# Optimization experiments

Hardware: AMD Instinct MI355X
Metric: run time of the kernel (lower is better)

The kernel has to match this reference:

```python
import jax, jax.numpy as jnp
import numpy as np

B, T = 256, 256
IN = [300, 74, 35]
H = [128, 32, 32]
TH = sum(H)            # 192 total hidden
ATT = 4                # attn_num
ACD = 64               # attn_cell_dim
COMP = [32, 16, 16]
ZDIM = sum(COMP)       # 64
CCD = [64, 32, 32]     # compression_cell_dims
OCD, OUT = 64, 1


def _mlp(x, w1, b1, w2, b2, act=None):
    # SimpleNet at inference: Linear -> ReLU -> (dropout=identity) -> Linear -> act
    o = jax.nn.relu(x @ w1 + b1) @ w2 + b2
    return act(o) if act is not None else o


def _lsthm(x, c, h, z, W, U, V, b, hd):
    s = x @ W + h @ U + z @ V + b  # [B, 4*hd]
    f = jax.nn.sigmoid(s[:, :hd])
    i = jax.nn.sigmoid(s[:, hd:2 * hd])
    o = jax.nn.sigmoid(s[:, 2 * hd:3 * hd])
    ch = jnp.tanh(s[:, 3 * hd:])
    c_t = f * c + i * ch
    h_t = jnp.tanh(c_t) * o
    return c_t, h_t


def setup_inputs() -> dict:
    key = jax.random.key(0)
    ks = iter(jax.random.split(key, 64))
    rn = lambda shape, s=0.05: jax.random.normal(next(ks), shape, dtype=jnp.float32) * s
    inp = {}
    for i, d in enumerate(IN):
        inp[f"x{i}"] = jax.random.normal(next(ks), (B, T, d), dtype=jnp.float32)
    for i in range(3):
        inp[f"W{i}"] = rn((IN[i], 4 * H[i]))
        inp[f"U{i}"] = rn((H[i], 4 * H[i]))
        inp[f"V{i}"] = rn((ZDIM, 4 * H[i]))
        inp[f"b{i}"] = jnp.zeros((4 * H[i],), jnp.float32)
    inp["aw1"] = rn((TH, ACD * ATT)); inp["ab1"] = jnp.zeros((ACD * ATT,), jnp.float32)
    inp["aw2"] = rn((ACD * ATT, TH * ATT)); inp["ab2"] = jnp.zeros((TH * ATT,), jnp.float32)
    for i in range(3):
        inp[f"cw1_{i}"] = rn((H[i] * ATT, CCD[i])); inp[f"cb1_{i}"] = jnp.zeros((CCD[i],), jnp.float32)
        inp[f"cw2_{i}"] = rn((CCD[i], COMP[i])); inp[f"cb2_{i}"] = jnp.zeros((COMP[i],), jnp.float32)
    inp["fw1"] = rn((ZDIM + TH, OCD)); inp["fb1"] = jnp.zeros((OCD,), jnp.float32)
    inp["fw2"] = rn((OCD, OUT)); inp["fb2"] = jnp.zeros((OUT,), jnp.float32)
    return inp


def reference(x0, x1, x2,
              W0, U0, V0, b0, W1, U1, V1, b1, W2, U2, V2, b2,
              aw1, ab1, aw2, ab2,
              cw1_0, cb1_0, cw2_0, cb2_0,
              cw1_1, cb1_1, cw2_1, cb2_1,
              cw1_2, cb1_2, cw2_2, cb2_2,
              fw1, fb1, fw2, fb2):
    b = x0.shape[0]
    init = (jnp.zeros((b, H[0]), x0.dtype), jnp.zeros((b, H[1]), x0.dtype), jnp.zeros((b, H[2]), x0.dtype),
            jnp.zeros((b, H[0]), x0.dtype), jnp.zeros((b, H[1]), x0.dtype), jnp.zeros((b, H[2]), x0.dtype),
            jnp.zeros((b, ZDIM), x0.dtype))
    s0 = H[0] * ATT
    s1 = s0 + H[1] * ATT

    def step(carry, xt):
        c0, c1, c2, h0, h1, h2, z = carry
        x0t, x1t, x2t = xt
        c0, h0 = _lsthm(x0t, c0, h0, z, W0, U0, V0, b0, H[0])
        c1, h1 = _lsthm(x1t, c1, h1, z, W1, U1, V1, b1, H[1])
        c2, h2 = _lsthm(x2t, c2, h2, z, W2, U2, V2, b2, H[2])
        hcat = jnp.concatenate([h0, h1, h2], axis=1)  # [B, TH]
        att = _mlp(hcat, aw1, ab1, aw2, ab2, jax.nn.sigmoid)  # [B, ATT*TH]
        atts = jax.nn.softmax(att.reshape(b, ATT, TH), axis=2).reshape(b, ATT * TH)
        out_tensor = jnp.concatenate([jnp.tile(h0, (1, ATT)), jnp.tile(h1, (1, ATT)), jnp.tile(h2, (1, ATT))], axis=1)
        att_out = atts * out_tensor
        d0 = _mlp(att_out[:, :s0], cw1_0, cb1_0, cw2_0, cb2_0, jax.nn.sigmoid)
        d1 = _mlp(att_out[:, s0:s1], cw1_1, cb1_1, cw2_1, cb2_1, jax.nn.sigmoid)
        d2 = _mlp(att_out[:, s1:], cw1_2, cb1_2, cw2_2, cb2_2, jax.nn.sigmoid)
        z = jax.nn.softmax(jnp.concatenate([d0, d1, d2], axis=1), axis=1)
        return (c0, c1, c2, h0, h1, h2, z), None

    xs = (jnp.swapaxes(x0, 0, 1), jnp.swapaxes(x1, 0, 1), jnp.swapaxes(x2, 0, 1))  # time-leading
    (c0, c1, c2, h0, h1, h2, z), _ = jax.lax.scan(step, init, xs)
    total = jnp.concatenate([z, h0, h1, h2], axis=1)  # [B, ZDIM+TH]
    return _mlp(total, fw1, fb1, fw2, fb2)  # [B, 1]
```

## Files before the change

### kernel.cpp

```cpp
#include <hip/hip_runtime.h>
#include <hip/hip_bf16.h>
#include <hip/hip_fp16.h>
#include <math.h>

#define BB 256
#define TT 256

__device__ __forceinline__ float sigf(float x) { return 1.f / (1.f + expf(-x)); }

typedef _Float16 half8v __attribute__((ext_vector_type(8)));
typedef _Float16 half2v __attribute__((ext_vector_type(2)));

__device__ __forceinline__ void dot8p(float (&acc)[8], float4 wv0, float4 wv1,
                                      float a0, float a1) {
#if __has_builtin(__builtin_amdgcn_fdot2)
    const half2v ap = __builtin_bit_cast(half2v, __builtin_amdgcn_cvt_pkrtz(a0, a1));
    acc[0] = __builtin_amdgcn_fdot2(__builtin_bit_cast(half2v, wv0.x), ap, acc[0], false);
    acc[1] = __builtin_amdgcn_fdot2(__builtin_bit_cast(half2v, wv0.y), ap, acc[1], false);
    acc[2] = __builtin_amdgcn_fdot2(__builtin_bit_cast(half2v, wv0.z), ap, acc[2], false);
    acc[3] = __builtin_amdgcn_fdot2(__builtin_bit_cast(half2v, wv0.w), ap, acc[3], false);
    acc[4] = __builtin_amdgcn_fdot2(__builtin_bit_cast(half2v, wv1.x), ap, acc[4], false);
    acc[5] = __builtin_amdgcn_fdot2(__builtin_bit_cast(half2v, wv1.y), ap, acc[5], false);
    acc[6] = __builtin_amdgcn_fdot2(__builtin_bit_cast(half2v, wv1.z), ap, acc[6], false);
    acc[7] = __builtin_amdgcn_fdot2(__builtin_bit_cast(half2v, wv1.w), ap, acc[7], false);
#else
    half8v h0 = __builtin_bit_cast(half8v, wv0);
    half8v h1 = __builtin_bit_cast(half8v, wv1);
#pragma unroll
    for (int m = 0; m < 4; ++m) acc[m]     += (float)h0[2*m] * a0 + (float)h0[2*m+1] * a1;
#pragma unroll
    for (int m = 0; m < 4; ++m) acc[4 + m] += (float)h1[2*m] * a0 + (float)h1[2*m+1] * a1;
#endif
}

#define BAR() do {                                   \
    __atomic_signal_fence(__ATOMIC_SEQ_CST);         \
    __builtin_amdgcn_s_waitcnt(0xC07F);              \
    __builtin_amdgcn_s_barrier();                    \
    __atomic_signal_fence(__ATOMIC_SEQ_CST);         \
} while (0)

__global__ void f2h_pair(const float* __restrict__ s, __half* __restrict__ d,
                         int K, int N) {
    int i = blockIdx.x * 256 + threadIdx.x;
    if (i < K * N) {
        int k = i / N, j = i - k * N;
        d[(size_t)(k >> 1) * (2 * N) + 2 * j + (k & 1)] = __float2half(s[i]);
    }
}

#define GT_M 128
#define GT_N 64
#define GT_K 16

__device__ __forceinline__ void stvec4(float* p, float4 v) { *(float4*)p = v; }
__device__ __forceinline__ void stvec4(__half* p, float4 v) {
    *(__half2*)p = __floats2half2_rn(v.x, v.y);
    *(__half2*)(p + 2) = __floats2half2_rn(v.z, v.w);
}

template <typename OT>
__global__ __launch_bounds__(256)
void xw_gemm(const float* __restrict__ X, const float* __restrict__ W,
             const float* __restrict__ bias, OT* __restrict__ G,
             int M, int N, int K) {
    __shared__ float As[GT_K][GT_M + 4];
    __shared__ float Bs[GT_K][GT_N];
    const int tid = threadIdx.x;
    const int bm = blockIdx.y * GT_M;
    const int bn = blockIdx.x * GT_N;
    const int tx = tid & 15;
    const int ty = tid >> 4;

    float acc[8][4];
#pragma unroll
    for (int i = 0; i < 8; ++i)
#pragma unroll
        for (int j = 0; j < 4; ++j) acc[i][j] = 0.f;

    for (int kt = 0; kt < K; kt += GT_K) {
#pragma unroll
        for (int i = 0; i < 8; ++i) {
            int idx = i * 256 + tid;
            int m = idx >> 4, k = idx & 15;
            int gk = kt + k;
            As[k][m] = (gk < K) ? X[(size_t)(bm + m) * K + gk] : 0.f;
        }
#pragma unroll
        for (int i = 0; i < 4; ++i) {
            int idx = i * 256 + tid;
            int k = idx >> 6, n = idx & 63;
            int gk = kt + k;
            Bs[k][n] = (gk < K) ? W[(size_t)gk * N + bn + n] : 0.f;
        }
        __syncthreads();
#pragma unroll
        for (int k = 0; k < GT_K; ++k) {
            float a[8], b[4];
            const float4 a0 = *(const float4*)&As[k][ty * 8];
            const float4 a1 = *(const float4*)&As[k][ty * 8 + 4];
            const float4 bv = *(const float4*)&Bs[k][tx * 4];
            a[0]=a0.x; a[1]=a0.y; a[2]=a0.z; a[3]=a0.w;
            a[4]=a1.x; a[5]=a1.y; a[6]=a1.z; a[7]=a1.w;
            b[0]=bv.x; b[1]=bv.y; b[2]=bv.z; b[3]=bv.w;
#pragma unroll
            for (int i = 0; i < 8; ++i)
#pragma unroll
                for (int j = 0; j < 4; ++j) acc[i][j] += a[i] * b[j];
        }
        __syncthreads();
    }
    const int n0 = bn + tx * 4;
#pragma unroll
    for (int i = 0; i < 8; ++i) {
        int m = bm + ty * 8 + i;
        float4 v;
        v.x = acc[i][0] + bias[n0 + 0];
        v.y = acc[i][1] + bias[n0 + 1];
        v.z = acc[i][2] + bias[n0 + 2];
        v.w = acc[i][3] + bias[n0 + 3];
        stvec4(&G[(size_t)m * N + n0], v);
    }
}

__global__ __launch_bounds__(512, 1)
void marn_rec(const float* __restrict__ G0, const __half* __restrict__ G1h,
              const __half* __restrict__ G2h,
              const __half* __restrict__ hU0, const __half* __restrict__ hV0,
              const __half* __restrict__ hU1, const __half* __restrict__ hV1,
              const __half* __restrict__ hU2, const __half* __restrict__ hV2,
              const __half* __restrict__ haw1, const float* __restrict__ ab1,
              const __half* __restrict__ haw2, const float* __restrict__ ab2,
              const __half* __restrict__ hcw10, const float* __restrict__ cb10,
              const float* __restrict__ cw20, const float* __restrict__ cb20,
              const __half* __restrict__ hcw11, const float* __restrict__ cb11,
              const float* __restrict__ cw21, const float* __restrict__ cb21,
              const __half* __restrict__ hcw12, const float* __restrict__ cb12,
              const float* __restrict__ cw22, const float* __restrict__ cb22,
              const float* __restrict__ fw1, const float* __restrict__ fb1,
              const float* __restrict__ fw2, const float* __restrict__ fb2,
              float* __restrict__ out) {
    __shared__ float hz[256];
    __shared__ float cst[192];
    __shared__ float a1s[256];
    __shared__ float attE[768];
    __shared__ float hid[128];
    __shared__ float rinv[4];
    __shared__ float scratch[3840];
    __shared__ float c2w[3072];
    __shared__ __align__(16) __half s_aw1[49152];
    __shared__ __align__(16) __half s_c1b[8192];

    const int tid = threadIdx.x;
    const int row = blockIdx.x;
    const int rotPA = ((row >> 3) & 3) * 4;
    const int rotPB = ((row >> 3) & 7) * 4;
    const int rotPC = ((row >> 3) & 3) * 4;

    for (int i = tid; i < 256; i += 512) hz[i] = 0.f;
    if (tid < 192) cst[tid] = 0.f;
    for (int i = tid; i < 2048; i += 512) c2w[i] = cw20[i];
    if (tid < 512) { c2w[2048 + tid] = cw21[tid]; c2w[2560 + tid] = cw22[tid]; }
    {
        const float4* s4 = (const float4*)haw1;
        float4* d4 = (float4*)s_aw1;
        for (int i = tid; i < 6144; i += 512) d4[i] = s4[i];
        float4* d1 = (float4*)s_c1b;
        d1[tid] = ((const float4*)hcw11)[tid];
        d1[512 + tid] = ((const float4*)hcw12)[tid];
    }
    __syncthreads();

    const __half* WBa = nullptr; int HOa = 0, STRa = 0, SOa = 0;
    if (tid < 384) {
        const int g = tid & 63, kc = tid >> 6;
        const int cb = g * 8;
        if (kc < 4) { WBa = hU0 + (size_t)(16 * kc) * 1024 + 2 * cb; HOa = 32 * kc; }
        else        { WBa = hV0 + (size_t)(16 * (kc - 4)) * 1024 + 2 * cb; HOa = 192 + 32 * (kc - 4); }
        STRa = 1024;
        SOa = kc * 512 + cb;
    } else if (tid < 480) {
        const int u = tid - 384;
        const int kc = u >> 5;
        const int g2 = u & 31;
        const int cell = g2 >> 4;
        const int cb = (g2 & 15) * 8;
        const __half* Uc = cell ? hU2 : hU1;
        const __half* Vc = cell ? hV2 : hV1;
        if (kc == 0) { WBa = Uc + 2 * cb; HOa = 128 + 32 * cell; }
        else         { WBa = Vc + (size_t)(16 * (kc - 1)) * 256 + 2 * cb; HOa = 192 + 32 * (kc - 1); }
        STRa = 256;
        SOa = 3072 + kc * 256 + cell * 128 + cb;
    }
    int AW1o = 0, HO1 = 0, SO1 = 0;
    if (tid < 256) {
        const int g = tid & 31, kc = tid >> 5;
        const int cb = g * 8;
        AW1o = kc * 6144 + 2 * cb;
        HO1 = 24 * kc;
        SO1 = kc * 256 + cb;
    }
    const int kc2 = tid / 96;
    const int g2a = tid - kc2 * 96;
    const __half* WB2 = haw2 + (size_t)(32 * kc2) * 1536 + 2 * (g2a * 8);
    const int HO2 = 64 * kc2;
    const int SO2 = kc2 * 768 + g2a * 8;
    const __half* WBc = nullptr; int HOc = 0, SOc = 0, C1o = 0, HSELo = 0, HSELm = 0, HBc = 0;
    if (tid < 128) {
        const int g = tid & 7, kc = tid >> 3;
        WBc = hcw10 + (size_t)(16 * kc) * 128 + 2 * (g * 8);
        HOc = 32 * kc;
        SOc = kc * 64 + g * 8;
        HSELo = 0; HSELm = 127; HBc = 0;
    } else if (tid < 192) {
        const int u = tid - 128;
        const int cell = u >> 5;
        const int rem = u & 31;
        const int g = rem & 3, kc = rem >> 2;
        C1o = cell * 4096 + kc * 512 + 2 * (g * 8);
        HOc = 512 + 128 * cell + 16 * kc;
        SOc = 1024 + cell * 256 + kc * 32 + g * 8;
        HSELo = 128 + 32 * cell; HSELm = 31; HBc = 512 + 128 * cell;
    }
    const int AHc = HOc / 192;
    const int g12_cell = ((tid - 128) >> 5) & 1;
    const int g12_uu   = (tid - 128) & 31;

    float  g0p[4];
    __half g12p[4];
    if (tid < 128) {
        const float* gp = G0 + ((size_t)row * TT + 0) * 512;
#pragma unroll
        for (int q = 0; q < 4; ++q) g0p[q] = gp[q * 128 + tid];
    } else if (tid < 192) {
        const __half* gp = (g12_cell ? G2h : G1h) + ((size_t)row * TT + 0) * 128;
#pragma unroll
        for (int q = 0; q < 4; ++q) g12p[q] = gp[q * 32 + g12_uu];
    }

    for (int t = 0; t < TT; ++t) {
        if (tid < 480) {
            float acc[8];
#pragma unroll
            for (int j = 0; j < 8; ++j) acc[j] = 0.f;
#pragma unroll 8
            for (int p = 0; p < 16; ++p) {
                const int kk = (p + rotPA) & 15;
                const __half* wp = WBa + (size_t)kk * STRa;
                dot8p(acc, *(const float4*)wp, *(const float4*)(wp + 8),
                      hz[HOa + 2 * kk], hz[HOa + 2 * kk + 1]);
            }
            float* s0 = &scratch[SOa];
            *(float4*)s0       = make_float4(acc[0], acc[1], acc[2], acc[3]);
            *(float4*)(s0 + 4) = make_float4(acc[4], acc[5], acc[6], acc[7]);
        }
        BAR();
        if (tid < 128) {
            float s[4];
#pragma unroll
            for (int q = 0; q < 4; ++q) {
                const int c4 = q * 128 + tid;
                float v = g0p[q];
#pragma unroll
                for (int kc = 0; kc < 6; ++kc) v += scratch[kc * 512 + c4];
                s[q] = v;
            }
            const float f  = sigf(s[0]);
            const float ig = sigf(s[1]);
            const float o  = sigf(s[2]);
            const float ch = tanhf(s[3]);
            const float c = f * cst[tid] + ig * ch;
            cst[tid] = c;
            hz[tid] = tanhf(c) * o;
        } else if (tid < 192) {
            const int cell = g12_cell, uu = g12_uu;
            float s[4];
#pragma unroll
            for (int q = 0; q < 4; ++q) {
                float v = __half2float(g12p[q]);
#pragma unroll
                for (int kc = 0; kc < 3; ++kc)
                    v += scratch[3072 + kc * 256 + cell * 128 + q * 32 + uu];
                s[q] = v;
            }
            const float f  = sigf(s[0]);
            const float ig = sigf(s[1]);
            const float o  = sigf(s[2]);
            const float ch = tanhf(s[3]);
            const int si = 128 + 32 * cell + uu;
            const float c = f * cst[si] + ig * ch;
            cst[si] = c;
            hz[si] = tanhf(c) * o;
        }
        BAR();
        if (tid < 256) {
            float acc[8];
#pragma unroll
            for (int j = 0; j < 8; ++j) acc[j] = 0.f;
            const __half* wp = &s_aw1[AW1o];
#pragma unroll
            for (int p = 0; p < 12; ++p)
                dot8p(acc, *(const float4*)(wp + p * 512), *(const float4*)(wp + p * 512 + 8),
                      hz[HO1 + 2 * p], hz[HO1 + 2 * p + 1]);
            float* s0 = &scratch[SO1];
            *(float4*)s0       = make_float4(acc[0], acc[1], acc[2], acc[3]);
            *(float4*)(s0 + 4) = make_float4(acc[4], acc[5], acc[6], acc[7]);
        }
        BAR();
        if (tid < 256) {
            float s = ab1[tid];
#pragma unroll
            for (int kc = 0; kc < 8; ++kc) s += scratch[kc * 256 + tid];
            a1s[tid] = fmaxf(s, 0.f);
        }
        BAR();
        if (tid < 384) {
            float acc[8];
#pragma unroll
            for (int j = 0; j < 8; ++j) acc[j] = 0.f;
#pragma unroll 8
            for (int p = 0; p < 32; ++p) {
                const int kk = (p + rotPB) & 31;
                const __half* wp = WB2 + (size_t)kk * 1536;
                dot8p(acc, *(const float4*)wp, *(const float4*)(wp + 8),
                      a1s[HO2 + 2 * kk], a1s[HO2 + 2 * kk + 1]);
            }
            float* s0 = &scratch[SO2];
            *(float4*)s0       = make_float4(acc[0], acc[1], acc[2], acc[3]);
            *(float4*)(s0 + 4) = make_float4(acc[4], acc[5], acc[6], acc[7]);
        }
        BAR();
#pragma unroll
        for (int i = 0; i < 2; ++i) {
            const int idx = i * 512 + tid;
            if (idx < 768) {
                float s = ab2[idx];
#pragma unroll
                for (int kc = 0; kc < 4; ++kc) s += scratch[kc * 768 + idx];
                attE[idx] = expf(sigf(s));
            }
        }
        BAR();
        if (tid < 256) {
            const int a = tid >> 6, lane = tid & 63;
            float v = attE[a * 192 + lane] + attE[a * 192 + 64 + lane]
                    + attE[a * 192 + 128 + lane];
#pragma unroll
            for (int s = 32; s >= 1; s >>= 1) v += __shfl_xor(v, s);
            if (lane == 0) rinv[a] = 1.f / v;
        }
        BAR();
        if (tid < 192) {
            const float ri = rinv[AHc];
            float acc[8];
#pragma unroll
            for (int j = 0; j < 8; ++j) acc[j] = 0.f;
            if (tid < 128) {
#pragma unroll 8
                for (int p = 0; p < 16; ++p) {
                    const int kk = (p + rotPC) & 15;
                    const int i0 = HOc + 2 * kk;
                    const float a0 = attE[i0] * ri * hz[i0 & 127];
                    const float a1 = attE[i0 + 1] * ri * hz[(i0 + 1) & 127];
                    const __half* wp = WBc + (size_t)kk * 128;
                    dot8p(acc, *(const float4*)wp, *(const float4*)(wp + 8), a0, a1);
                }
            } else {
                const __half* wp = &s_c1b[C1o];
#pragma unroll
                for (int p = 0; p < 8; ++p) {
                    const int i0 = HOc + 2 * p;
                    const float a0 = attE[i0] * ri * hz[HSELo + ((i0 - HBc) & HSELm)];
                    const float a1 = attE[i0 + 1] * ri * hz[HSELo + ((i0 + 1 - HBc) & HSELm)];
                    dot8p(acc, *(const float4*)(wp + p * 64), *(const float4*)(wp + p * 64 + 8),
                          a0, a1);
                }
            }
            float* s0 = &scratch[SOc];
            *(float4*)s0       = make_float4(acc[0], acc[1], acc[2], acc[3]);
            *(float4*)(s0 + 4) = make_float4(acc[4], acc[5], acc[6], acc[7]);
        }
        BAR();
        if (tid < 128) {
            float s;
            if (tid < 64) {
                s = cb10[tid];
#pragma unroll
                for (int kc = 0; kc < 16; ++kc) s += scratch[kc * 64 + tid];
            } else {
                const int cc = tid - 64;
                const int cell = cc >> 5, j = cc & 31;
                s = (cell ? cb12 : cb11)[j];
#pragma unroll
                for (int kc = 0; kc < 8; ++kc)
                    s += scratch[1024 + cell * 256 + kc * 32 + j];
            }
            hid[tid] = fmaxf(s, 0.f);
        }
        BAR();
        if (tid < 64) {
            const int j = tid;
            float acc;
            if (j < 32) {
                acc = cb20[j];
#pragma unroll
                for (int k = 0; k < 64; ++k) acc += hid[k] * c2w[k * 32 + j];
            } else if (j < 48) {
                const int o = j - 32; acc = cb21[o];
#pragma unroll
                for (int k = 0; k < 32; ++k) acc += hid[64 + k] * c2w[2048 + k * 16 + o];
            } else {
                const int o = j - 48; acc = cb22[o];
#pragma unroll
                for (int k = 0; k < 32; ++k) acc += hid[96 + k] * c2w[2560 + k * 16 + o];
            }
            const float e = expf(sigf(acc));
            float v = e;
#pragma unroll
            for (int s = 32; s >= 1; s >>= 1) v += __shfl_xor(v, s);
            hz[192 + j] = e / v;
        }
        {
            const int tn = (t + 1 < TT) ? t + 1 : TT - 1;
            if (tid < 128) {
                const float* gp = G0 + ((size_t)row * TT + tn) * 512;
#pragma unroll
                for (int q = 0; q < 4; ++q) g0p[q] = gp[q * 128 + tid];
            } else if (tid < 192) {
                const __half* gp = (g12_cell ? G2h : G1h) + ((size_t)row * TT + tn) * 128;
#pragma unroll
                for (int q = 0; q < 4; ++q) g12p[q] = gp[q * 32 + g12_uu];
            }
        }
        BAR();
    }

    __syncthreads();
    if (tid < 64) {
        const int j = tid;
        float acc = fb1[j];
#pragma unroll 8
        for (int k = 0; k < 64; ++k)  acc += hz[192 + k] * fw1[k * 64 + j];
#pragma unroll 8
        for (int k = 0; k < 192; ++k) acc += hz[k] * fw1[(64 + k) * 64 + j];
        hid[j] = fmaxf(acc, 0.f);
    }
    __syncthreads();
    if (tid < 64) {
        float v = hid[tid] * fw2[tid];
#pragma unroll
        for (int s = 32; s >= 1; s >>= 1) v += __shfl_xor(v, s);
        if (tid == 0) out[row] = v + fb2[0];
    }
}

extern "C" void kernel_launch(void* const* d_in, const int* in_sizes, int n_in,
                              void* d_out, int out_size, void* d_ws, size_t ws_size,
                              hipStream_t stream) {
    const float* x0   = (const float*)d_in[0];
    const float* x1   = (const float*)d_in[1];
    const float* x2   = (const float*)d_in[2];
    const float* W0   = (const float*)d_in[3];
    const float* U0   = (const float*)d_in[4];
    const float* V0   = (const float*)d_in[5];
    const float* b0   = (const float*)d_in[6];
    const float* W1   = (const float*)d_in[7];
    const float* U1   = (const float*)d_in[8];
    const float* V1   = (const float*)d_in[9];
    const float* b1   = (const float*)d_in[10];
    const float* W2   = (const float*)d_in[11];
    const float* U2   = (const float*)d_in[12];
    const float* V2   = (const float*)d_in[13];
    const float* b2   = (const float*)d_in[14];
    const float* aw1  = (const float*)d_in[15];
    const float* ab1  = (const float*)d_in[16];
    const float* aw2  = (const float*)d_in[17];
    const float* ab2  = (const float*)d_in[18];
    const float* cw10 = (const float*)d_in[19];
    const float* cb10 = (const float*)d_in[20];
    const float* cw20 = (const float*)d_in[21];
    const float* cb20 = (const float*)d_in[22];
    const float* cw11 = (const float*)d_in[23];
    const float* cb11 = (const float*)d_in[24];
    const float* cw21 = (const float*)d_in[25];
    const float* cb21 = (const float*)d_in[26];
    const float* cw12 = (const float*)d_in[27];
    const float* cb12 = (const float*)d_in[28];
    const float* cw22 = (const float*)d_in[29];
    const float* cb22 = (const float*)d_in[30];
    const float* fw1  = (const float*)d_in[31];
    const float* fb1  = (const float*)d_in[32];
    const float* fw2  = (const float*)d_in[33];
    const float* fb2  = (const float*)d_in[34];
    float* out = (float*)d_out;

    const size_t M = (size_t)BB * TT;

    float*  G0  = (float*)d_ws;
    __half* G1h = (__half*)(G0 + M * 512);
    __half* G2h = G1h + M * 128;
    __half* hU0   = G2h + M * 128;
    __half* hV0   = hU0 + 65536;
    __half* hU1   = hV0 + 32768;
    __half* hV1   = hU1 + 4096;
    __half* hU2   = hV1 + 8192;
    __half* hV2   = hU2 + 4096;
    __half* haw1  = hV2 + 8192;
    __half* haw2  = haw1 + 49152;
    __half* hcw10 = haw2 + 196608;
    __half* hcw11 = hcw10 + 32768;
    __half* hcw12 = hcw11 + 4096;

    f2h_pair<<<(65536 + 255) / 256, 256, 0, stream>>>(U0, hU0, 128, 512);
    f2h_pair<<<(32768 + 255) / 256, 256, 0, stream>>>(V0, hV0, 64, 512);
    f2h_pair<<<(4096 + 255) / 256, 256, 0, stream>>>(U1, hU1, 32, 128);
    f2h_pair<<<(8192 + 255) / 256, 256, 0, stream>>>(V1, hV1, 64, 128);
    f2h_pair<<<(4096 + 255) / 256, 256, 0, stream>>>(U2, hU2, 32, 128);
    f2h_pair<<<(8192 + 255) / 256, 256, 0, stream>>>(V2, hV2, 64, 128);
    f2h_pair<<<(49152 + 255) / 256, 256, 0, stream>>>(aw1, haw1, 192, 256);
    f2h_pair<<<(196608 + 255) / 256, 256, 0, stream>>>(aw2, haw2, 256, 768);
    f2h_pair<<<(32768 + 255) / 256, 256, 0, stream>>>(cw10, hcw10, 512, 64);
    f2h_pair<<<(4096 + 255) / 256, 256, 0, stream>>>(cw11, hcw11, 128, 32);
    f2h_pair<<<(4096 + 255) / 256, 256, 0, stream>>>(cw12, hcw12, 128, 32);

    xw_gemm<float><<<dim3(512 / GT_N, M / GT_M), 256, 0, stream>>>(x0, W0, b0, G0, (int)M, 512, 300);
    xw_gemm<__half><<<dim3(128 / GT_N, M / GT_M), 256, 0, stream>>>(x1, W1, b1, G1h, (int)M, 128, 74);
    xw_gemm<__half><<<dim3(128 / GT_N, M / GT_M), 256, 0, stream>>>(x2, W2, b2, G2h, (int)M, 128, 35);

    marn_rec<<<256, 512, 0, stream>>>(G0, G1h, G2h, hU0, hV0, hU1, hV1, hU2, hV2,
                                      haw1, ab1, haw2, ab2,
                                      hcw10, cb10, cw20, cb20,
                                      hcw11, cb11, cw21, cb21,
                                      hcw12, cb12, cw22, cb22,
                                      fw1, fb1, fw2, fb2, out);
}
```

Before: 3.202 ms.

## Overlap U0 recurrent matvec with attention stage and defer softmax normalization

Moves the h0·U0 partial products out of the first per-step phase and into the idle threads of the attention first-layer phase, storing them in a new shared buffer for the next step's gate sum. The softmax normalization is deferred: the compression layer uses unnormalized exponentials and the per-head reciprocal is applied afterward per k-chunk, which lets the row-sum reduction run concurrently with the compression matvec and removes one barrier per timestep. This costs extra shared memory and relies on each k-chunk mapping to exactly one attention head.

```diff
diff --git a/kernel.cpp b/kernel.cpp
--- a/kernel.cpp
+++ b/kernel.cpp
@@ -146,6 +146,7 @@
     __shared__ float attE[768];
     __shared__ float hid[128];
     __shared__ float rinv[4];
+    __shared__ float uhA[2048];
     __shared__ float scratch[3840];
     __shared__ float c2w[3072];
     __shared__ __align__(16) __half s_aw1[49152];
@@ -159,6 +160,7 @@
 
     for (int i = tid; i < 256; i += 512) hz[i] = 0.f;
     if (tid < 192) cst[tid] = 0.f;
+    for (int i = tid; i < 2048; i += 512) uhA[i] = 0.f;
     for (int i = tid; i < 2048; i += 512) c2w[i] = cw20[i];
     if (tid < 512) { c2w[2048 + tid] = cw21[tid]; c2w[2560 + tid] = cw22[tid]; }
     {
@@ -192,6 +194,12 @@
         STRa = 256;
         SOa = 3072 + kc * 256 + cell * 128 + cb;
     }
+    const int uj   = tid - 256;
+    const int ukc  = (uj >> 6) & 3;
+    const int ug   = uj & 63;
+    const __half* WBu = hU0 + (size_t)(16 * ukc) * 1024 + 2 * (ug * 8);
+    const int HOu = 32 * ukc;
+    const int UOu = ukc * 512 + ug * 8;
     int AW1o = 0, HO1 = 0, SO1 = 0;
     if (tid < 256) {
         const int g = tid & 31, kc = tid >> 5;
@@ -222,7 +230,6 @@
         SOc = 1024 + cell * 256 + kc * 32 + g * 8;
         HSELo = 128 + 32 * cell; HSELm = 31; HBc = 512 + 128 * cell;
     }
-    const int AHc = HOc / 192;
     const int g12_cell = ((tid - 128) >> 5) & 1;
     const int g12_uu   = (tid - 128) & 31;
 
@@ -239,7 +246,7 @@
     }
 
     for (int t = 0; t < TT; ++t) {
-        if (tid < 480) {
+        if (tid >= 256 && tid < 480) {
             float acc[8];
 #pragma unroll
             for (int j = 0; j < 8; ++j) acc[j] = 0.f;
@@ -262,7 +269,9 @@
                 const int c4 = q * 128 + tid;
                 float v = g0p[q];
 #pragma unroll
-                for (int kc = 0; kc < 6; ++kc) v += scratch[kc * 512 + c4];
+                for (int kc = 0; kc < 4; ++kc) v += uhA[kc * 512 + c4];
+#pragma unroll
+                for (int kc = 4; kc < 6; ++kc) v += scratch[kc * 512 + c4];
                 s[q] = v;
             }
             const float f  = sigf(s[0]);
@@ -305,6 +314,20 @@
             float* s0 = &scratch[SO1];
             *(float4*)s0       = make_float4(acc[0], acc[1], acc[2], acc[3]);
             *(float4*)(s0 + 4) = make_float4(acc[4], acc[5], acc[6], acc[7]);
+        } else {
+            float acc[8];
+#pragma unroll
+            for (int j = 0; j < 8; ++j) acc[j] = 0.f;
+#pragma unroll 8
+            for (int p = 0; p < 16; ++p) {
+                const int kk = (p + rotPA) & 15;
+                const __half* wp = WBu + (size_t)kk * 1024;
+                dot8p(acc, *(const float4*)wp, *(const float4*)(wp + 8),
+                      hz[HOu + 2 * kk], hz[HOu + 2 * kk + 1]);
+            }
+            float* s0 = &uhA[UOu];
+            *(float4*)s0       = make_float4(acc[0], acc[1], acc[2], acc[3]);
+            *(float4*)(s0 + 4) = make_float4(acc[4], acc[5], acc[6], acc[7]);
         }
         BAR();
         if (tid < 256) {
@@ -341,17 +364,7 @@
             }
         }
         BAR();
-        if (tid < 256) {
-            const int a = tid >> 6, lane = tid & 63;
-            float v = attE[a * 192 + lane] + attE[a * 192 + 64 + lane]
-                    + attE[a * 192 + 128 + lane];
-#pragma unroll
-            for (int s = 32; s >= 1; s >>= 1) v += __shfl_xor(v, s);
-            if (lane == 0) rinv[a] = 1.f / v;
-        }
-        BAR();
         if (tid < 192) {
-            const float ri = rinv[AHc];
             float acc[8];
 #pragma unroll
             for (int j = 0; j < 8; ++j) acc[j] = 0.f;
@@ -360,8 +373,8 @@
                 for (int p = 0; p < 16; ++p) {
                     const int kk = (p + rotPC) & 15;
                     const int i0 = HOc + 2 * kk;
-                    const float a0 = attE[i0] * ri * hz[i0 & 127];
-                    const float a1 = attE[i0 + 1] * ri * hz[(i0 + 1) & 127];
+                    const float a0 = attE[i0] * hz[i0 & 127];
+                    const float a1 = attE[i0 + 1] * hz[(i0 + 1) & 127];
                     const __half* wp = WBc + (size_t)kk * 128;
                     dot8p(acc, *(const float4*)wp, *(const float4*)(wp + 8), a0, a1);
                 }
@@ -370,8 +383,8 @@
 #pragma unroll
                 for (int p = 0; p < 8; ++p) {
                     const int i0 = HOc + 2 * p;
-                    const float a0 = attE[i0] * ri * hz[HSELo + ((i0 - HBc) & HSELm)];
-                    const float a1 = attE[i0 + 1] * ri * hz[HSELo + ((i0 + 1 - HBc) & HSELm)];
+                    const float a0 = attE[i0] * hz[HSELo + ((i0 - HBc) & HSELm)];
+                    const float a1 = attE[i0 + 1] * hz[HSELo + ((i0 + 1 - HBc) & HSELm)];
                     dot8p(acc, *(const float4*)(wp + p * 64), *(const float4*)(wp + p * 64 + 8),
                           a0, a1);
                 }
@@ -379,6 +392,14 @@
             float* s0 = &scratch[SOc];
             *(float4*)s0       = make_float4(acc[0], acc[1], acc[2], acc[3]);
             *(float4*)(s0 + 4) = make_float4(acc[4], acc[5], acc[6], acc[7]);
+        } else if (tid < 448) {
+            const int u = tid - 192;
+            const int a = u >> 6, lane = u & 63;
+            float v = attE[a * 192 + lane] + attE[a * 192 + 64 + lane]
+                    + attE[a * 192 + 128 + lane];
+#pragma unroll
+            for (int s = 32; s >= 1; s >>= 1) v += __shfl_xor(v, s);
+            if (lane == 0) rinv[a] = 1.f / v;
         }
         BAR();
         if (tid < 128) {
@@ -386,14 +407,16 @@
             if (tid < 64) {
                 s = cb10[tid];
 #pragma unroll
-                for (int kc = 0; kc < 16; ++kc) s += scratch[kc * 64 + tid];
+                for (int kc = 0; kc < 16; ++kc)
+                    s += scratch[kc * 64 + tid] * rinv[(32 * kc) / 192];
             } else {
                 const int cc = tid - 64;
                 const int cell = cc >> 5, j = cc & 31;
                 s = (cell ? cb12 : cb11)[j];
 #pragma unroll
                 for (int kc = 0; kc < 8; ++kc)
-                    s += scratch[1024 + cell * 256 + kc * 32 + j];
+                    s += scratch[1024 + cell * 256 + kc * 32 + j]
+                         * rinv[(512 + 128 * cell + 16 * kc) / 192];
             }
             hid[tid] = fmaxf(s, 0.f);
         }
```

New measurement: 3.257 ms. No clear change (+1.7%).

## Process two batch rows per block to reuse recurrent weight loads

Applied to the files above, without the earlier changes.

Each workgroup now handles two batch rows, duplicating hidden state, scratch and attention buffers, and each loaded weight vector feeds two accumulator sets. The grid is halved to 128 blocks. The aim is to halve per-row weight fetch bandwidth and put idle threads to work in the elementwise phases. The risk is longer per-timestep latency in a sequential recurrence and leaving half the CUs unused. The LDS copy of the small compression weights is also removed, so those are now read from global memory.

```diff
diff --git a/kernel.cpp b/kernel.cpp
--- a/kernel.cpp
+++ b/kernel.cpp
@@ -140,34 +140,31 @@
               const float* __restrict__ fw1, const float* __restrict__ fb1,
               const float* __restrict__ fw2, const float* __restrict__ fb2,
               float* __restrict__ out) {
-    __shared__ float hz[256];
-    __shared__ float cst[192];
-    __shared__ float a1s[256];
-    __shared__ float attE[768];
-    __shared__ float hid[128];
-    __shared__ float rinv[4];
-    __shared__ float scratch[3840];
+    __shared__ float hz[512];
+    __shared__ float cst[384];
+    __shared__ float a1s[512];
+    __shared__ float attE[1536];
+    __shared__ float hid[256];
+    __shared__ float rinv[8];
+    __shared__ float scratch[7680];
     __shared__ float c2w[3072];
     __shared__ __align__(16) __half s_aw1[49152];
-    __shared__ __align__(16) __half s_c1b[8192];
 
     const int tid = threadIdx.x;
-    const int row = blockIdx.x;
-    const int rotPA = ((row >> 3) & 3) * 4;
-    const int rotPB = ((row >> 3) & 7) * 4;
-    const int rotPC = ((row >> 3) & 3) * 4;
-
-    for (int i = tid; i < 256; i += 512) hz[i] = 0.f;
-    if (tid < 192) cst[tid] = 0.f;
+    const int bid = blockIdx.x;
+    const int row0 = 2 * bid;
+    const int rotPA = ((bid >> 3) & 3) * 4;
+    const int rotPB = ((bid >> 3) & 7) * 4;
+    const int rotPC = ((bid >> 3) & 3) * 4;
+
+    hz[tid] = 0.f;
+    if (tid < 384) cst[tid] = 0.f;
     for (int i = tid; i < 2048; i += 512) c2w[i] = cw20[i];
-    if (tid < 512) { c2w[2048 + tid] = cw21[tid]; c2w[2560 + tid] = cw22[tid]; }
+    { c2w[2048 + tid] = cw21[tid & 511]; c2w[2560 + tid] = cw22[tid & 511]; }
     {
         const float4* s4 = (const float4*)haw1;
         float4* d4 = (float4*)s_aw1;
         for (int i = tid; i < 6144; i += 512) d4[i] = s4[i];
-        float4* d1 = (float4*)s_c1b;
-        d1[tid] = ((const float4*)hcw11)[tid];
-        d1[512 + tid] = ((const float4*)hcw12)[tid];
     }
     __syncthreads();
 
@@ -192,108 +189,122 @@
         STRa = 256;
         SOa = 3072 + kc * 256 + cell * 128 + cb;
     }
-    int AW1o = 0, HO1 = 0, SO1 = 0;
-    if (tid < 256) {
-        const int g = tid & 31, kc = tid >> 5;
-        const int cb = g * 8;
-        AW1o = kc * 6144 + 2 * cb;
+    const int lt = tid & 255;
+    const int rr = tid >> 8;
+    int AW1o, HO1, SO1;
+    {
+        const int g = lt & 31, kc = lt >> 5;
+        AW1o = kc * 6144 + 2 * (g * 8);
         HO1 = 24 * kc;
-        SO1 = kc * 256 + cb;
+        SO1 = kc * 256 + g * 8;
     }
     const int kc2 = tid / 96;
     const int g2a = tid - kc2 * 96;
     const __half* WB2 = haw2 + (size_t)(32 * kc2) * 1536 + 2 * (g2a * 8);
     const int HO2 = 64 * kc2;
     const int SO2 = kc2 * 768 + g2a * 8;
-    const __half* WBc = nullptr; int HOc = 0, SOc = 0, C1o = 0, HSELo = 0, HSELm = 0, HBc = 0;
+    const __half* WBc = nullptr; const __half* WC1 = nullptr;
+    int HOc = 0, SOc = 0, HSELo = 0, HSELm = 0, HBc = 0, AHc = 0, c1row = 0;
     if (tid < 128) {
         const int g = tid & 7, kc = tid >> 3;
         WBc = hcw10 + (size_t)(16 * kc) * 128 + 2 * (g * 8);
         HOc = 32 * kc;
         SOc = kc * 64 + g * 8;
-        HSELo = 0; HSELm = 127; HBc = 0;
-    } else if (tid < 192) {
-        const int u = tid - 128;
+        AHc = HOc / 192;
+    } else if (tid < 256) {
+        const int u = (tid - 128) & 63;
+        c1row = (tid - 128) >> 6;
         const int cell = u >> 5;
         const int rem = u & 31;
         const int g = rem & 3, kc = rem >> 2;
-        C1o = cell * 4096 + kc * 512 + 2 * (g * 8);
+        WC1 = (cell ? hcw12 : hcw11) + kc * 512 + 2 * (g * 8);
         HOc = 512 + 128 * cell + 16 * kc;
         SOc = 1024 + cell * 256 + kc * 32 + g * 8;
         HSELo = 128 + 32 * cell; HSELm = 31; HBc = 512 + 128 * cell;
-    }
-    const int AHc = HOc / 192;
-    const int g12_cell = ((tid - 128) >> 5) & 1;
-    const int g12_uu   = (tid - 128) & 31;
+        AHc = HOc / 192;
+    }
+    const bool gBig   = (tid < 128) || (tid >= 256 && tid < 384);
+    const bool gSmall = (lt >= 128 && lt < 192);
+    const int  gC     = tid & 127;
+    const int  sCell  = ((lt - 128) >> 5) & 1;
+    const int  sUU    = (lt - 128) & 31;
 
     float  g0p[4];
     __half g12p[4];
-    if (tid < 128) {
-        const float* gp = G0 + ((size_t)row * TT + 0) * 512;
-#pragma unroll
-        for (int q = 0; q < 4; ++q) g0p[q] = gp[q * 128 + tid];
-    } else if (tid < 192) {
-        const __half* gp = (g12_cell ? G2h : G1h) + ((size_t)row * TT + 0) * 128;
-#pragma unroll
-        for (int q = 0; q < 4; ++q) g12p[q] = gp[q * 32 + g12_uu];
+    if (gBig) {
+        const float* gp = G0 + ((size_t)(row0 + rr) * TT + 0) * 512;
+#pragma unroll
+        for (int q = 0; q < 4; ++q) g0p[q] = gp[q * 128 + gC];
+    } else if (gSmall) {
+        const __half* gp = (sCell ? G2h : G1h) + ((size_t)(row0 + rr) * TT + 0) * 128;
+#pragma unroll
+        for (int q = 0; q < 4; ++q) g12p[q] = gp[q * 32 + sUU];
     }
 
     for (int t = 0; t < TT; ++t) {
         if (tid < 480) {
-            float acc[8];
-#pragma unroll
-            for (int j = 0; j < 8; ++j) acc[j] = 0.f;
+            float acc0[8], acc1[8];
+#pragma unroll
+            for (int j = 0; j < 8; ++j) { acc0[j] = 0.f; acc1[j] = 0.f; }
 #pragma unroll 8
             for (int p = 0; p < 16; ++p) {
                 const int kk = (p + rotPA) & 15;
                 const __half* wp = WBa + (size_t)kk * STRa;
-                dot8p(acc, *(const float4*)wp, *(const float4*)(wp + 8),
-                      hz[HOa + 2 * kk], hz[HOa + 2 * kk + 1]);
+                const float4 wv0 = *(const float4*)wp;
+                const float4 wv1 = *(const float4*)(wp + 8);
+                dot8p(acc0, wv0, wv1, hz[HOa + 2 * kk], hz[HOa + 2 * kk + 1]);
+                dot8p(acc1, wv0, wv1, hz[256 + HOa + 2 * kk], hz[256 + HOa + 2 * kk + 1]);
             }
             float* s0 = &scratch[SOa];
-            *(float4*)s0       = make_float4(acc[0], acc[1], acc[2], acc[3]);
-            *(float4*)(s0 + 4) = make_float4(acc[4], acc[5], acc[6], acc[7]);
-        }
-        BAR();
-        if (tid < 128) {
+            *(float4*)s0       = make_float4(acc0[0], acc0[1], acc0[2], acc0[3]);
+            *(float4*)(s0 + 4) = make_float4(acc0[4], acc0[5], acc0[6], acc0[7]);
+            float* s1 = &scratch[3840 + SOa];
+            *(float4*)s1       = make_float4(acc1[0], acc1[1], acc1[2], acc1[3]);
+            *(float4*)(s1 + 4) = make_float4(acc1[4], acc1[5], acc1[6], acc1[7]);
+        }
+        BAR();
+        if (gBig) {
+            const float* scr = scratch + rr * 3840;
             float s[4];
 #pragma unroll
             for (int q = 0; q < 4; ++q) {
-                const int c4 = q * 128 + tid;
+                const int c4 = q * 128 + gC;
                 float v = g0p[q];
 #pragma unroll
-                for (int kc = 0; kc < 6; ++kc) v += scratch[kc * 512 + c4];
+                for (int kc = 0; kc < 6; ++kc) v += scr[kc * 512 + c4];
                 s[q] = v;
             }
             const float f  = sigf(s[0]);
             const float ig = sigf(s[1]);
             const float o  = sigf(s[2]);
             const float ch = tanhf(s[3]);
-            const float c = f * cst[tid] + ig * ch;
-            cst[tid] = c;
-            hz[tid] = tanhf(c) * o;
-        } else if (tid < 192) {
-            const int cell = g12_cell, uu = g12_uu;
+            const int ci = rr * 192 + gC;
+            const float c = f * cst[ci] + ig * ch;
+            cst[ci] = c;
+            hz[rr * 256 + gC] = tanhf(c) * o;
+        } else if (gSmall) {
+            const float* scr = scratch + rr * 3840;
             float s[4];
 #pragma unroll
             for (int q = 0; q < 4; ++q) {
                 float v = __half2float(g12p[q]);
 #pragma unroll
                 for (int kc = 0; kc < 3; ++kc)
-                    v += scratch[3072 + kc * 256 + cell * 128 + q * 32 + uu];
+                    v += scr[3072 + kc * 256 + sCell * 128 + q * 32 + sUU];
                 s[q] = v;
             }
             const float f  = sigf(s[0]);
             const float ig = sigf(s[1]);
             const float o  = sigf(s[2]);
             const float ch = tanhf(s[3]);
-            const int si = 128 + 32 * cell + uu;
-            const float c = f * cst[si] + ig * ch;
-            cst[si] = c;
-            hz[si] = tanhf(c) * o;
-        }
-        BAR();
-        if (tid < 256) {
+            const int si = 128 + 32 * sCell + sUU;
+            const float c = f * cst[rr * 192 + si] + ig * ch;
+            cst[rr * 192 + si] = c;
+            hz[rr * 256 + si] = tanhf(c) * o;
+        }
+        BAR();
+        {
+            const float* hzB = hz + rr * 256;
             float acc[8];
 #pragma unroll
             for (int j = 0; j < 8; ++j) acc[j] = 0.f;
@@ -301,33 +312,39 @@
 #pragma unroll
             for (int p = 0; p < 12; ++p)
                 dot8p(acc, *(const float4*)(wp + p * 512), *(const float4*)(wp + p * 512 + 8),
-                      hz[HO1 + 2 * p], hz[HO1 + 2 * p + 1]);
-            float* s0 = &scratch[SO1];
+                      hzB[HO1 + 2 * p], hzB[HO1 + 2 * p + 1]);
+            float* s0 = &scratch[rr * 3840 + SO1];
             *(float4*)s0       = make_float4(acc[0], acc[1], acc[2], acc[3]);
             *(float4*)(s0 + 4) = make_float4(acc[4], acc[5], acc[6], acc[7]);
         }
         BAR();
-        if (tid < 256) {
-            float s = ab1[tid];
-#pragma unroll
-            for (int kc = 0; kc < 8; ++kc) s += scratch[kc * 256 + tid];
-            a1s[tid] = fmaxf(s, 0.f);
+        {
+            const float* scr = scratch + rr * 3840;
+            float s = ab1[lt];
+#pragma unroll
+            for (int kc = 0; kc < 8; ++kc) s += scr[kc * 256 + lt];
+            a1s[rr * 256 + lt] = fmaxf(s, 0.f);
         }
         BAR();
         if (tid < 384) {
-            float acc[8];
-#pragma unroll
-            for (int j = 0; j < 8; ++j) acc[j] = 0.f;
+            float acc0[8], acc1[8];
+#pragma unroll
+            for (int j = 0; j < 8; ++j) { acc0[j] = 0.f; acc1[j] = 0.f; }
 #pragma unroll 8
             for (int p = 0; p < 32; ++p) {
                 const int kk = (p + rotPB) & 31;
                 const __half* wp = WB2 + (size_t)kk * 1536;
-                dot8p(acc, *(const float4*)wp, *(const float4*)(wp + 8),
-                      a1s[HO2 + 2 * kk], a1s[HO2 + 2 * kk + 1]);
+                const float4 wv0 = *(const float4*)wp;
+                const float4 wv1 = *(const float4*)(wp + 8);
+                dot8p(acc0, wv0, wv1, a1s[HO2 + 2 * kk], a1s[HO2 + 2 * kk + 1]);
+                dot8p(acc1, wv0, wv1, a1s[256 + HO2 + 2 * kk], a1s[256 + HO2 + 2 * kk + 1]);
             }
             float* s0 = &scratch[SO2];
-            *(float4*)s0       = make_float4(acc[0], acc[1], acc[2], acc[3]);
-            *(float4*)(s0 + 4) = make_float4(acc[4], acc[5], acc[6], acc[7]);
+            *(float4*)s0       = make_float4(acc0[0], acc0[1], acc0[2], acc0[3]);
+            *(float4*)(s0 + 4) = make_float4(acc0[4], acc0[5], acc0[6], acc0[7]);
+            float* s1 = &scratch[3840 + SO2];
+            *(float4*)s1       = make_float4(acc1[0], acc1[1], acc1[2], acc1[3]);
+            *(float4*)(s1 + 4) = make_float4(acc1[4], acc1[5], acc1[6], acc1[7]);
         }
         BAR();
 #pragma unroll
@@ -340,117 +357,146 @@
                 attE[idx] = expf(sigf(s));
             }
         }
-        BAR();
-        if (tid < 256) {
-            const int a = tid >> 6, lane = tid & 63;
-            float v = attE[a * 192 + lane] + attE[a * 192 + 64 + lane]
-                    + attE[a * 192 + 128 + lane];
+#pragma unroll
+        for (int i = 0; i < 2; ++i) {
+            const int idx = i * 512 + tid;
+            if (idx < 768) {
+                float s = ab2[idx];
+#pragma unroll
+                for (int kc = 0; kc < 4; ++kc) s += scratch[3840 + kc * 768 + idx];
+                attE[768 + idx] = expf(sigf(s));
+            }
+        }
+        BAR();
+        {
+            const int a = lt >> 6, lane = lt & 63;
+            const float* aE = attE + rr * 768;
+            float v = aE[a * 192 + lane] + aE[a * 192 + 64 + lane]
+                    + aE[a * 192 + 128 + lane];
 #pragma unroll
             for (int s = 32; s >= 1; s >>= 1) v += __shfl_xor(v, s);
-            if (lane == 0) rinv[a] = 1.f / v;
-        }
-        BAR();
-        if (tid < 192) {
-            const float ri = rinv[AHc];
+            if (lane == 0) rinv[rr * 4 + a] = 1.f / v;
+        }
+        BAR();
+        if (tid < 128) {
+            const float ri0 = rinv[AHc], ri1 = rinv[4 + AHc];
+            float acc0[8], acc1[8];
+#pragma unroll
+            for (int j = 0; j < 8; ++j) { acc0[j] = 0.f; acc1[j] = 0.f; }
+#pragma unroll 8
+            for (int p = 0; p < 16; ++p) {
+                const int kk = (p + rotPC) & 15;
+                const int i0 = HOc + 2 * kk;
+                const float a00 = attE[i0] * ri0 * hz[i0 & 127];
+                const float a01 = attE[i0 + 1] * ri0 * hz[(i0 + 1) & 127];
+                const float a10 = attE[768 + i0] * ri1 * hz[256 + (i0 & 127)];
+                const float a11 = attE[768 + i0 + 1] * ri1 * hz[256 + ((i0 + 1) & 127)];
+                const __half* wp = WBc + (size_t)kk * 128;
+                const float4 wv0 = *(const float4*)wp;
+                const float4 wv1 = *(const float4*)(wp + 8);
+                dot8p(acc0, wv0, wv1, a00, a01);
+                dot8p(acc1, wv0, wv1, a10, a11);
+            }
+            float* s0 = &scratch[SOc];
+            *(float4*)s0       = make_float4(acc0[0], acc0[1], acc0[2], acc0[3]);
+            *(float4*)(s0 + 4) = make_float4(acc0[4], acc0[5], acc0[6], acc0[7]);
+            float* s1 = &scratch[3840 + SOc];
+            *(float4*)s1       = make_float4(acc1[0], acc1[1], acc1[2], acc1[3]);
+            *(float4*)(s1 + 4) = make_float4(acc1[4], acc1[5], acc1[6], acc1[7]);
+        } else if (tid < 256) {
+            const float ri = rinv[c1row * 4 + AHc];
+            const float* aE = attE + c1row * 768;
+            const float* hzB = hz + c1row * 256;
             float acc[8];
 #pragma unroll
             for (int j = 0; j < 8; ++j) acc[j] = 0.f;
-            if (tid < 128) {
-#pragma unroll 8
-                for (int p = 0; p < 16; ++p) {
-                    const int kk = (p + rotPC) & 15;
-                    const int i0 = HOc + 2 * kk;
-                    const float a0 = attE[i0] * ri * hz[i0 & 127];
-                    const float a1 = attE[i0 + 1] * ri * hz[(i0 + 1) & 127];
-                    const __half* wp = WBc + (size_t)kk * 128;
-                    dot8p(acc, *(const float4*)wp, *(const float4*)(wp + 8), a0, a1);
-                }
-            } else {
-                const __half* wp = &s_c1b[C1o];
-#pragma unroll
-                for (int p = 0; p < 8; ++p) {
-                    const int i0 = HOc + 2 * p;
-                    const float a0 = attE[i0] * ri * hz[HSELo + ((i0 - HBc) & HSELm)];
-                    const float a1 = attE[i0 + 1] * ri * hz[HSELo + ((i0 + 1 - HBc) & HSELm)];
-                    dot8p(acc, *(const float4*)(wp + p * 64), *(const float4*)(wp + p * 64 + 8),
-                          a0, a1);
-                }
-            }
-            float* s0 = &scratch[SOc];
+#pragma unroll
+            for (int p = 0; p < 8; ++p) {
+                const int i0 = HOc + 2 * p;
+                const float a0 = aE[i0] * ri * hzB[HSELo + ((i0 - HBc) & HSELm)];
+                const float a1 = aE[i0 + 1] * ri * hzB[HSELo + ((i0 + 1 - HBc) & HSELm)];
+                const __half* wp = WC1 + p * 64;
+                dot8p(acc, *(const float4*)wp, *(const float4*)(wp + 8), a0, a1);
+            }
+            float* s0 = &scratch[c1row * 3840 + SOc];
             *(float4*)s0       = make_float4(acc[0], acc[1], acc[2], acc[3]);
             *(float4*)(s0 + 4) = make_float4(acc[4], acc[5], acc[6], acc[7]);
         }
         BAR();
-        if (tid < 128) {
+        if (gBig) {
+            const float* scr = scratch + rr * 3840;
             float s;
-            if (tid < 64) {
-                s = cb10[tid];
-#pragma unroll
-                for (int kc = 0; kc < 16; ++kc) s += scratch[kc * 64 + tid];
+            if (gC < 64) {
+                s = cb10[gC];
+#pragma unroll
+                for (int kc = 0; kc < 16; ++kc) s += scr[kc * 64 + gC];
             } else {
-                const int cc = tid - 64;
+                const int cc = gC - 64;
                 const int cell = cc >> 5, j = cc & 31;
                 s = (cell ? cb12 : cb11)[j];
 #pragma unroll
                 for (int kc = 0; kc < 8; ++kc)
-                    s += scratch[1024 + cell * 256 + kc * 32 + j];
-            }
-            hid[tid] = fmaxf(s, 0.f);
-        }
-        BAR();
-        if (tid < 64) {
-            const int j = tid;
+                    s += scr[1024 + cell * 256 + kc * 32 + j];
+            }
+            hid[rr * 128 + gC] = fmaxf(s, 0.f);
+        }
+        BAR();
+        if (tid < 64 || (tid >= 256 && tid < 320)) {
+            const int j = tid & 63;
+            const float* hb = hid + rr * 128;
             float acc;
             if (j < 32) {
                 acc = cb20[j];
 #pragma unroll
-                for (int k = 0; k < 64; ++k) acc += hid[k] * c2w[k * 32 + j];
+                for (int k = 0; k < 64; ++k) acc += hb[k] * c2w[k * 32 + j];
             } else if (j < 48) {
                 const int o = j - 32; acc = cb21[o];
 #pragma unroll
-                for (int k = 0; k < 32; ++k) acc += hid[64 + k] * c2w[2048 + k * 16 + o];
+                for (int k = 0; k < 32; ++k) acc += hb[64 + k] * c2w[2048 + k * 16 + o];
             } else {
                 const int o = j - 48; acc = cb22[o];
 #pragma unroll
-                for (int k = 0; k < 32; ++k) acc += hid[96 + k] * c2w[2560 + k * 16 + o];
+                for (int k = 0; k < 32; ++k) acc += hb[96 + k] * c2w[2560 + k * 16 + o];
             }
             const float e = expf(sigf(acc));
             float v = e;
 #pragma unroll
             for (int s = 32; s >= 1; s >>= 1) v += __shfl_xor(v, s);
-            hz[192 + j] = e / v;
+            hz[rr * 256 + 192 + j] = e / v;
         }
         {
             const int tn = (t + 1 < TT) ? t + 1 : TT - 1;
-            if (tid < 128) {
-                const float* gp = G0 + ((size_t)row * TT + tn) * 512;
-#pragma unroll
-                for (int q = 0; q < 4; ++q) g0p[q] = gp[q * 128 + tid];
-            } else if (tid < 192) {
-                const __half* gp = (g12_cell ? G2h : G1h) + ((size_t)row * TT + tn) * 128;
-#pragma unroll
-                for (int q = 0; q < 4; ++q) g12p[q] = gp[q * 32 + g12_uu];
+            if (gBig) {
+                const float* gp = G0 + ((size_t)(row0 + rr) * TT + tn) * 512;
+#pragma unroll
+                for (int q = 0; q < 4; ++q) g0p[q] = gp[q * 128 + gC];
+            } else if (gSmall) {
+                const __half* gp = (sCell ? G2h : G1h) + ((size_t)(row0 + rr) * TT + tn) * 128;
+#pragma unroll
+                for (int q = 0; q < 4; ++q) g12p[q] = gp[q * 32 + sUU];
             }
         }
         BAR();
     }
 
     __syncthreads();
-    if (tid < 64) {
-        const int j = tid;
+    if (tid < 64 || (tid >= 256 && tid < 320)) {
+        const int j = tid & 63;
+        const float* hzB = hz + rr * 256;
         float acc = fb1[j];
 #pragma unroll 8
-        for (int k = 0; k < 64; ++k)  acc += hz[192 + k] * fw1[k * 64 + j];
+        for (int k = 0; k < 64; ++k)  acc += hzB[192 + k] * fw1[k * 64 + j];
 #pragma unroll 8
-        for (int k = 0; k < 192; ++k) acc += hz[k] * fw1[(64 + k) * 64 + j];
-        hid[j] = fmaxf(acc, 0.f);
+        for (int k = 0; k < 192; ++k) acc += hzB[k] * fw1[(64 + k) * 64 + j];
+        hid[rr * 128 + j] = fmaxf(acc, 0.f);
     }
     __syncthreads();
-    if (tid < 64) {
-        float v = hid[tid] * fw2[tid];
+    if (tid < 64 || (tid >= 256 && tid < 320)) {
+        const int j = tid & 63;
+        float v = hid[rr * 128 + j] * fw2[j];
 #pragma unroll
         for (int s = 32; s >= 1; s >>= 1) v += __shfl_xor(v, s);
-        if (tid == 0) out[row] = v + fb2[0];
+        if (j == 0) out[row0 + rr] = v + fb2[0];
     }
 }
 
@@ -527,7 +573,7 @@
     xw_gemm<__half><<<dim3(128 / GT_N, M / GT_M), 256, 0, stream>>>(x1, W1, b1, G1h, (int)M, 128, 74);
     xw_gemm<__half><<<dim3(128 / GT_N, M / GT_M), 256, 0, stream>>>(x2, W2, b2, G2h, (int)M, 128, 35);
 
-    marn_rec<<<256, 512, 0, stream>>>(G0, G1h, G2h, hU0, hV0, hU1, hV1, hU2, hV2,
+    marn_rec<<<128, 512, 0, stream>>>(G0, G1h, G2h, hU0, hV0, hU1, hV1, hU2, hV2,
                                       haw1, ab1, haw2, ab2,
                                       hcw10, cb10, cw20, cb20,
                                       hcw11, cb11, cw21, cb21,
```

New measurement: 3.857 ms. 1.2x slower.
